# Performance work log

Hardware: AMD Instinct MI355X
Metric: run time of the kernel (lower is better)

## Reference

```python
import jax, jax.numpy as jnp
import numpy as np

PROCESSING_STEPS = 3


def setup_inputs() -> dict:
    key = jax.random.key(0)
    ks = jax.random.split(key, 6)
    N, D, G = 500000, 128, 4096
    x = jax.random.normal(ks[0], (N, D), dtype=jnp.float32)
    # torch LSTM param layout: [4*hidden, input] and [4*hidden, hidden], gates i,f,g,o
    s = 1.0 / np.sqrt(D)
    W_ih = jax.random.uniform(ks[1], (4 * D, 2 * D), minval=-s, maxval=s, dtype=jnp.float32)
    W_hh = jax.random.uniform(ks[2], (4 * D, D), minval=-s, maxval=s, dtype=jnp.float32)
    b_ih = jax.random.uniform(ks[3], (4 * D,), minval=-s, maxval=s, dtype=jnp.float32)
    b_hh = jax.random.uniform(ks[4], (4 * D,), minval=-s, maxval=s, dtype=jnp.float32)
    index = jnp.sort(jax.random.randint(ks[5], (N,), 0, G, dtype=jnp.int64))
    return {"x": x, "W_ih": W_ih, "W_hh": W_hh, "b_ih": b_ih, "b_hh": b_hh,
            "index": index, "dim_size": G}


def _lstm_cell(inp, h, c, W_ih, W_hh, b_ih, b_hh):
    gates = inp @ W_ih.T + h @ W_hh.T + (b_ih + b_hh)  # [G, 4D]
    i, f, g, o = jnp.split(gates, 4, axis=-1)
    c = jax.nn.sigmoid(f) * c + jax.nn.sigmoid(i) * jnp.tanh(g)
    h = jax.nn.sigmoid(o) * jnp.tanh(c)
    return h, c


def reference(x, W_ih, W_hh, b_ih, b_hh, index, dim_size):
    N, D = x.shape
    h = jnp.zeros((dim_size, D), dtype=x.dtype)
    c = jnp.zeros((dim_size, D), dtype=x.dtype)
    q_star = jnp.zeros((dim_size, 2 * D), dtype=x.dtype)
    for _ in range(PROCESSING_STEPS):
        h, c = _lstm_cell(q_star, h, c, W_ih, W_hh, b_ih, b_hh)
        q = h  # [G, D]
        e = jnp.sum(x * q[index], axis=-1)  # [N]
        # segment softmax (numerically stable)
        m = jax.ops.segment_max(e, index, num_segments=dim_size)
        m = jnp.where(jnp.isfinite(m), m, 0.0)  # guard empty segments
        ex = jnp.exp(e - m[index])
        s = jax.ops.segment_sum(ex, index, num_segments=dim_size)
        a = ex / jnp.maximum(s, 1e-16)[index]  # [N]
        r = jax.ops.segment_sum(a[:, None] * x, index, num_segments=dim_size)  # [G, D]
        q_star = jnp.concatenate([q, r], axis=-1)
    return q_star
```

## Files before the change

### kernel.cpp

```cpp
#include <hip/hip_runtime.h>
#include <math.h>

#define D 128

__device__ __forceinline__ float sigmoidf_(float x) { return 1.f / (1.f + __expf(-x)); }

__global__ void seg_bounds_kernel(const int* __restrict__ idx, int N, int G,
                                  int* __restrict__ seg_off) {
    int g = blockIdx.x * blockDim.x + threadIdx.x;
    if (g > G) return;
    int lo = 0, hi = N;
    while (lo < hi) {
        int mid = (lo + hi) >> 1;
        if (idx[mid] < g) lo = mid + 1; else hi = mid;
    }
    seg_off[g] = lo;
}

__global__ void prep_wc_kernel(const float* __restrict__ W_ih, const float* __restrict__ W_hh,
                               float* __restrict__ Wc) {
    int t = blockIdx.x * blockDim.x + threadIdx.x;
    if (t >= 4 * D * D) return;
    int j = t >> 7;
    int k = t & (D - 1);
    Wc[t] = W_ih[(size_t)j * (2 * D) + k] + W_hh[t];
}

__global__ void prep_bias_kernel(const float* __restrict__ b_ih, const float* __restrict__ b_hh,
                                 float* __restrict__ b_sum, float* __restrict__ h1,
                                 float* __restrict__ c1) {
    int t = threadIdx.x;
    float b = b_ih[t] + b_hh[t];
    b_sum[t] = b;
    if (t < D) {
        float bi = b_ih[t] + b_hh[t];
        float bg = b_ih[2 * D + t] + b_hh[2 * D + t];
        float bo = b_ih[3 * D + t] + b_hh[3 * D + t];
        float c = sigmoidf_(bi) * tanhf(bg);
        c1[t] = c;
        h1[t] = sigmoidf_(bo) * tanhf(c);
    }
}

__global__ void base2_kernel(const float* __restrict__ Wc, const float* __restrict__ b_sum,
                             const float* __restrict__ h1, float* __restrict__ base2) {
    __shared__ float hs[D];
    int j = blockIdx.x * 256 + threadIdx.x;
    if (threadIdx.x < D) hs[threadIdx.x] = h1[threadIdx.x];
    __syncthreads();
    float acc = 0.f;
    const float4* w4 = (const float4*)(Wc + (size_t)j * D);
#pragma unroll 8
    for (int k4 = 0; k4 < D / 4; ++k4) {
        float4 w = w4[k4];
        const float* hp = &hs[k4 * 4];
        acc += w.x * hp[0] + w.y * hp[1] + w.z * hp[2] + w.w * hp[3];
    }
    base2[j] = b_sum[j] + acc;
}

__global__ __launch_bounds__(256) void attn_kernel(
    const float* __restrict__ x,
    const int* __restrict__ seg_off,
    const float* __restrict__ q,
    int q_stride,
    float* __restrict__ r_out, int r_stride,
    int G) {
    int g = blockIdx.x;
    if (g >= G) return;
    int tid = threadIdx.x;
    int wave = tid >> 6, lane = tid & 63;
    int half = lane >> 5, col4 = lane & 31;

    __shared__ float sm[4], ss[4];
    __shared__ float sacc[4][D];

    int start = seg_off[g], end = seg_off[g + 1];
    int count = end - start;
    int chunk = (count + 3) >> 2;
    int wsr = start + wave * chunk;
    int wer = min(wsr + chunk, end);

    const float4* x4 = (const float4*)x;
    const float4* q4 = (const float4*)(q + (size_t)g * q_stride);
    float4 qv = q4[col4];

    float m = -INFINITY, s = 0.f;
    float4 acc = {0.f, 0.f, 0.f, 0.f};

    if (wsr < wer) {
        int last = wer - 1;
        int ngroups = (wer - wsr + 7) >> 3;
        for (int it = 0; it < ngroups; ++it) {
            int base = wsr + it * 8;
            int ra = min(base + 0 + half, last);
            int rb = min(base + 2 + half, last);
            int rc = min(base + 4 + half, last);
            int rd = min(base + 6 + half, last);
            float4 xa = x4[(size_t)ra * 32 + col4];
            float4 xb = x4[(size_t)rb * 32 + col4];
            float4 xc = x4[(size_t)rc * 32 + col4];
            float4 xd = x4[(size_t)rd * 32 + col4];

            float pa = xa.x * qv.x + xa.y * qv.y + xa.z * qv.z + xa.w * qv.w;
            float pb = xb.x * qv.x + xb.y * qv.y + xb.z * qv.z + xb.w * qv.w;
            float pc = xc.x * qv.x + xc.y * qv.y + xc.z * qv.z + xc.w * qv.w;
            float pd = xd.x * qv.x + xd.y * qv.y + xd.z * qv.z + xd.w * qv.w;
#pragma unroll
            for (int off = 1; off < 32; off <<= 1) {
                pa += __shfl_xor(pa, off);
                pb += __shfl_xor(pb, off);
                pc += __shfl_xor(pc, off);
                pd += __shfl_xor(pd, off);
            }
            float oa = __shfl_xor(pa, 32);
            float ob = __shfl_xor(pb, 32);
            float oc = __shfl_xor(pc, 32);
            float od = __shfl_xor(pd, 32);
            float pae = half ? oa : pa, pao = half ? pa : oa;
            float pbe = half ? ob : pb, pbo = half ? pb : ob;
            float pce = half ? oc : pc, pco = half ? pc : oc;
            float pde = half ? od : pd, pdo = half ? pd : od;
            pae = (base + 0 < wer) ? pae : -INFINITY;
            pao = (base + 1 < wer) ? pao : -INFINITY;
            pbe = (base + 2 < wer) ? pbe : -INFINITY;
            pbo = (base + 3 < wer) ? pbo : -INFINITY;
            pce = (base + 4 < wer) ? pce : -INFINITY;
            pco = (base + 5 < wer) ? pco : -INFINITY;
            pde = (base + 6 < wer) ? pde : -INFINITY;
            pdo = (base + 7 < wer) ? pdo : -INFINITY;

            float mn = fmaxf(fmaxf(fmaxf(pae, pao), fmaxf(pbe, pbo)),
                             fmaxf(fmaxf(pce, pco), fmaxf(pde, pdo)));
            mn = fmaxf(m, mn);
            float al = __expf(m - mn);
            float wae = __expf(pae - mn), wao = __expf(pao - mn);
            float wbe = __expf(pbe - mn), wbo = __expf(pbo - mn);
            float wce = __expf(pce - mn), wco = __expf(pco - mn);
            float wde = __expf(pde - mn), wdo = __expf(pdo - mn);
            float sg = (wae + wao) + (wbe + wbo) + ((wce + wco) + (wde + wdo));
            s = s * al + sg;
            float wsa = half ? wao : wae;
            float wsb = half ? wbo : wbe;
            float wsc = half ? wco : wce;
            float wsd = half ? wdo : wde;
            float tx = wsa * xa.x + wsb * xb.x + wsc * xc.x + wsd * xd.x;
            float ty = wsa * xa.y + wsb * xb.y + wsc * xc.y + wsd * xd.y;
            float tz = wsa * xa.z + wsb * xb.z + wsc * xc.z + wsd * xd.z;
            float tw = wsa * xa.w + wsb * xb.w + wsc * xc.w + wsd * xd.w;
            acc.x = acc.x * al + tx;
            acc.y = acc.y * al + ty;
            acc.z = acc.z * al + tz;
            acc.w = acc.w * al + tw;
            m = mn;
        }
    }
    acc.x += __shfl_xor(acc.x, 32);
    acc.y += __shfl_xor(acc.y, 32);
    acc.z += __shfl_xor(acc.z, 32);
    acc.w += __shfl_xor(acc.w, 32);

    if (lane == 0) { sm[wave] = m; ss[wave] = s; }
    if (half == 0) *(float4*)&sacc[wave][col4 * 4] = acc;
    __syncthreads();

    if (tid < D) {
        float m0 = sm[0], m1 = sm[1], m2 = sm[2], m3 = sm[3];
        float mstar = fmaxf(fmaxf(m0, m1), fmaxf(m2, m3));
        float r = 0.f;
        if (mstar > -INFINITY) {
            float e0 = __expf(m0 - mstar), e1 = __expf(m1 - mstar);
            float e2 = __expf(m2 - mstar), e3 = __expf(m3 - mstar);
            float stot = ss[0] * e0 + ss[1] * e1 + ss[2] * e2 + ss[3] * e3;
            float at = sacc[0][tid] * e0 + sacc[1][tid] * e1
                     + sacc[2][tid] * e2 + sacc[3][tid] * e3;
            r = at / fmaxf(stot, 1e-16f);
        }
        r_out[(size_t)g * r_stride + tid] = r;
    }
}

__global__ __launch_bounds__(256) void gates_gemm_kernel(
    const float* __restrict__ A1, const float* __restrict__ W1,
    const float* __restrict__ A2, const float* __restrict__ W2, int sW2,
    const float* __restrict__ bias, float* __restrict__ gates) {
    __shared__ float As[16][132];
    __shared__ float Ws[16][132];
    int t = threadIdx.x;
    int tx = t & 15, ty = t >> 4;
    int g0 = blockIdx.x * 128, j0 = blockIdx.y * 128;
    int lr = t >> 1;
    int lk = (t & 1) * 8;

    float acc[8][8];
#pragma unroll
    for (int i = 0; i < 8; ++i)
#pragma unroll
        for (int j = 0; j < 8; ++j) acc[i][j] = 0.f;

    for (int phase = 0; phase < 2; ++phase) {
        const float* A = phase ? A2 : A1;
        if (A == nullptr) continue;
        const float* W = phase ? W2 : W1;
        int sW = phase ? sW2 : D;
        for (int kk = 0; kk < D; kk += 16) {
            float4 a0 = *(const float4*)&A[(size_t)(g0 + lr) * D + kk + lk];
            float4 a1 = *(const float4*)&A[(size_t)(g0 + lr) * D + kk + lk + 4];
            float4 w0 = *(const float4*)&W[(size_t)(j0 + lr) * sW + kk + lk];
            float4 w1 = *(const float4*)&W[(size_t)(j0 + lr) * sW + kk + lk + 4];
            __syncthreads();
            As[lk + 0][lr] = a0.x; As[lk + 1][lr] = a0.y; As[lk + 2][lr] = a0.z; As[lk + 3][lr] = a0.w;
            As[lk + 4][lr] = a1.x; As[lk + 5][lr] = a1.y; As[lk + 6][lr] = a1.z; As[lk + 7][lr] = a1.w;
            Ws[lk + 0][lr] = w0.x; Ws[lk + 1][lr] = w0.y; Ws[lk + 2][lr] = w0.z; Ws[lk + 3][lr] = w0.w;
            Ws[lk + 4][lr] = w1.x; Ws[lk + 5][lr] = w1.y; Ws[lk + 6][lr] = w1.z; Ws[lk + 7][lr] = w1.w;
            __syncthreads();
#pragma unroll
            for (int k = 0; k < 16; ++k) {
                float4 a0v = *(const float4*)&As[k][ty * 8];
                float4 a1v = *(const float4*)&As[k][ty * 8 + 4];
                float4 b0v = *(const float4*)&Ws[k][tx * 8];
                float4 b1v = *(const float4*)&Ws[k][tx * 8 + 4];
                float av[8] = {a0v.x, a0v.y, a0v.z, a0v.w, a1v.x, a1v.y, a1v.z, a1v.w};
                float bv[8] = {b0v.x, b0v.y, b0v.z, b0v.w, b1v.x, b1v.y, b1v.z, b1v.w};
#pragma unroll
                for (int i = 0; i < 8; ++i)
#pragma unroll
                    for (int j = 0; j < 8; ++j)
                        acc[i][j] = fmaf(av[i], bv[j], acc[i][j]);
            }
        }
    }
#pragma unroll
    for (int i = 0; i < 8; ++i) {
        size_t row = (size_t)(g0 + ty * 8 + i);
        float4 o0, o1;
        int jb = j0 + tx * 8;
        o0.x = acc[i][0] + bias[jb + 0]; o0.y = acc[i][1] + bias[jb + 1];
        o0.z = acc[i][2] + bias[jb + 2]; o0.w = acc[i][3] + bias[jb + 3];
        o1.x = acc[i][4] + bias[jb + 4]; o1.y = acc[i][5] + bias[jb + 5];
        o1.z = acc[i][6] + bias[jb + 6]; o1.w = acc[i][7] + bias[jb + 7];
        *(float4*)&gates[row * 512 + jb] = o0;
        *(float4*)&gates[row * 512 + jb + 4] = o1;
    }
}

__global__ void cell_kernel(const float* __restrict__ gates,
                            const float* __restrict__ c_prev, int c_stride,
                            float* __restrict__ c_out,
                            float* __restrict__ h_out, int h_stride,
                            int total) {
    int t = blockIdx.x * blockDim.x + threadIdx.x;
    if (t >= total) return;
    int g = t >> 7, k = t & (D - 1);
    const float* grow = gates + (size_t)g * 512;
    float ig = grow[k];
    float fg = grow[D + k];
    float gg = grow[2 * D + k];
    float og = grow[3 * D + k];
    float cp = c_prev[(size_t)g * c_stride + k];
    float c = sigmoidf_(fg) * cp + sigmoidf_(ig) * tanhf(gg);
    float h = sigmoidf_(og) * tanhf(c);
    c_out[t] = c;
    h_out[(size_t)g * h_stride + k] = h;
}

extern "C" void kernel_launch(void* const* d_in, const int* in_sizes, int n_in,
                              void* d_out, int out_size, void* d_ws, size_t ws_size,
                              hipStream_t stream) {
    const float* x      = (const float*)d_in[0];
    const float* W_ih   = (const float*)d_in[1];
    const float* W_hh   = (const float*)d_in[2];
    const float* b_ih   = (const float*)d_in[3];
    const float* b_hh   = (const float*)d_in[4];
    const int*   index  = (const int*)d_in[5];
    int N = in_sizes[5];
    int G = out_size / (2 * D);
    float* out = (float*)d_out;

    float* ws = (float*)d_ws;
    float* Wc     = ws;
    float* b_sum  = Wc + 4 * D * D;
    float* h1     = b_sum + 4 * D;
    float* c1     = h1 + D;
    float* base2  = c1 + D;
    float* r1     = base2 + 4 * D;
    float* h2     = r1 + (size_t)G * D;
    float* c2     = h2 + (size_t)G * D;
    float* r2     = c2 + (size_t)G * D;
    float* gatesb = r2 + (size_t)G * D;
    int* seg_off  = (int*)(gatesb + (size_t)G * 4 * D);
    float* c3     = r1;

    seg_bounds_kernel<<<(G + 1 + 255) / 256, 256, 0, stream>>>(index, N, G, seg_off);
    prep_wc_kernel<<<(4 * D * D + 255) / 256, 256, 0, stream>>>(W_ih, W_hh, Wc);
    prep_bias_kernel<<<1, 512, 0, stream>>>(b_ih, b_hh, b_sum, h1, c1);
    base2_kernel<<<2, 256, 0, stream>>>(Wc, b_sum, h1, base2);

    attn_kernel<<<G, 256, 0, stream>>>(x, seg_off, h1, 0, r1, D, G);

    gates_gemm_kernel<<<dim3(G / 128, 4), 256, 0, stream>>>(
        nullptr, Wc, r1, W_ih + D, 2 * D, base2, gatesb);
    cell_kernel<<<(G * D + 255) / 256, 256, 0, stream>>>(gatesb, c1, 0, c2, h2, D, G * D);
    attn_kernel<<<G, 256, 0, stream>>>(x, seg_off, h2, D, r2, D, G);

    gates_gemm_kernel<<<dim3(G / 128, 4), 256, 0, stream>>>(
        h2, Wc, r2, W_ih + D, 2 * D, b_sum, gatesb);
    cell_kernel<<<(G * D + 255) / 256, 256, 0, stream>>>(gatesb, c2, D, c3, out, 2 * D, G * D);
    attn_kernel<<<G, 256, 0, stream>>>(x, seg_off, out, 2 * D, out + D, 2 * D, G);
}
```

Baseline: 523.1 us.

## Fuse prep kernels into one launch and shrink gates GEMM tiles to 64x64

Merges the segment-bounds, combined-weight, and bias/initial-state kernels into one prep kernel, so fewer launches happen. It drops the precomputed base2 vector and instead runs the first-step GEMM with a broadcast h1 row (stride 0), which adds a small amount of GEMM work. The gates GEMM moves from 128x128 tiles with 8x8 per-thread to 64x64 tiles with 4x4 per-thread and K-step 32, giving 4x more blocks for better CU occupancy on 4096 rows at the cost of lower register-level reuse.

```diff
diff --git a/kernel.cpp b/kernel.cpp
--- a/kernel.cpp
+++ b/kernel.cpp
@@ -5,67 +5,44 @@
 
 __device__ __forceinline__ float sigmoidf_(float x) { return 1.f / (1.f + __expf(-x)); }
 
-__global__ void seg_bounds_kernel(const int* __restrict__ idx, int N, int G,
-                                  int* __restrict__ seg_off) {
-    int g = blockIdx.x * blockDim.x + threadIdx.x;
-    if (g > G) return;
-    int lo = 0, hi = N;
-    while (lo < hi) {
-        int mid = (lo + hi) >> 1;
-        if (idx[mid] < g) lo = mid + 1; else hi = mid;
-    }
-    seg_off[g] = lo;
-}
-
-__global__ void prep_wc_kernel(const float* __restrict__ W_ih, const float* __restrict__ W_hh,
-                               float* __restrict__ Wc) {
-    int t = blockIdx.x * blockDim.x + threadIdx.x;
-    if (t >= 4 * D * D) return;
-    int j = t >> 7;
-    int k = t & (D - 1);
-    Wc[t] = W_ih[(size_t)j * (2 * D) + k] + W_hh[t];
-}
-
-__global__ void prep_bias_kernel(const float* __restrict__ b_ih, const float* __restrict__ b_hh,
-                                 float* __restrict__ b_sum, float* __restrict__ h1,
-                                 float* __restrict__ c1) {
-    int t = threadIdx.x;
-    float b = b_ih[t] + b_hh[t];
-    b_sum[t] = b;
-    if (t < D) {
-        float bi = b_ih[t] + b_hh[t];
-        float bg = b_ih[2 * D + t] + b_hh[2 * D + t];
-        float bo = b_ih[3 * D + t] + b_hh[3 * D + t];
-        float c = sigmoidf_(bi) * tanhf(bg);
-        c1[t] = c;
-        h1[t] = sigmoidf_(bo) * tanhf(c);
-    }
-}
-
-__global__ void base2_kernel(const float* __restrict__ Wc, const float* __restrict__ b_sum,
-                             const float* __restrict__ h1, float* __restrict__ base2) {
-    __shared__ float hs[D];
-    int j = blockIdx.x * 256 + threadIdx.x;
-    if (threadIdx.x < D) hs[threadIdx.x] = h1[threadIdx.x];
-    __syncthreads();
-    float acc = 0.f;
-    const float4* w4 = (const float4*)(Wc + (size_t)j * D);
-#pragma unroll 8
-    for (int k4 = 0; k4 < D / 4; ++k4) {
-        float4 w = w4[k4];
-        const float* hp = &hs[k4 * 4];
-        acc += w.x * hp[0] + w.y * hp[1] + w.z * hp[2] + w.w * hp[3];
-    }
-    base2[j] = b_sum[j] + acc;
+__global__ void prep_kernel(const float* __restrict__ W_ih, const float* __restrict__ W_hh,
+                            const float* __restrict__ b_ih, const float* __restrict__ b_hh,
+                            const int* __restrict__ idx, int N, int G,
+                            float* __restrict__ Wc, int* __restrict__ seg_off,
+                            float* __restrict__ b_sum, float* __restrict__ h1,
+                            float* __restrict__ c1) {
+    int b = blockIdx.x, t = threadIdx.x;
+    if (b < 256) {
+        int i = b * 256 + t;
+        int j = i >> 7, k = i & (D - 1);
+        Wc[i] = W_ih[(size_t)j * (2 * D) + k] + W_hh[i];
+    } else if (b < 273) {
+        int g = (b - 256) * 256 + t;
+        if (g <= G) {
+            int lo = 0, hi = N;
+            while (lo < hi) {
+                int mid = (lo + hi) >> 1;
+                if (idx[mid] < g) lo = mid + 1; else hi = mid;
+            }
+            seg_off[g] = lo;
+        }
+    } else {
+        for (int i = t; i < 4 * D; i += 256) b_sum[i] = b_ih[i] + b_hh[i];
+        if (t < D) {
+            float bi = b_ih[t] + b_hh[t];
+            float bg = b_ih[2 * D + t] + b_hh[2 * D + t];
+            float bo = b_ih[3 * D + t] + b_hh[3 * D + t];
+            float c = sigmoidf_(bi) * tanhf(bg);
+            c1[t] = c;
+            h1[t] = sigmoidf_(bo) * tanhf(c);
+        }
+    }
 }
 
 __global__ __launch_bounds__(256) void attn_kernel(
-    const float* __restrict__ x,
-    const int* __restrict__ seg_off,
-    const float* __restrict__ q,
-    int q_stride,
-    float* __restrict__ r_out, int r_stride,
-    int G) {
+    const float* __restrict__ x, const int* __restrict__ seg_off,
+    const float* __restrict__ q, int q_stride,
+    float* __restrict__ r_out, int r_stride, int G) {
     int g = blockIdx.x;
     if (g >= G) return;
     int tid = threadIdx.x;
@@ -181,31 +158,34 @@
 }
 
 __global__ __launch_bounds__(256) void gates_gemm_kernel(
-    const float* __restrict__ A1, const float* __restrict__ W1,
-    const float* __restrict__ A2, const float* __restrict__ W2, int sW2,
-    const float* __restrict__ bias, float* __restrict__ gates) {
-    __shared__ float As[16][132];
-    __shared__ float Ws[16][132];
+    const float* __restrict__ A1, int sA1,
+    const float* __restrict__ W1,
+    const float* __restrict__ A2,
+    const float* __restrict__ W2, int sW2,
+    const float* __restrict__ bias,
+    float* __restrict__ gates) {
+    __shared__ float As[32][72];
+    __shared__ float Ws[32][72];
     int t = threadIdx.x;
     int tx = t & 15, ty = t >> 4;
-    int g0 = blockIdx.x * 128, j0 = blockIdx.y * 128;
-    int lr = t >> 1;
-    int lk = (t & 1) * 8;
-
-    float acc[8][8];
-#pragma unroll
-    for (int i = 0; i < 8; ++i)
-#pragma unroll
-        for (int j = 0; j < 8; ++j) acc[i][j] = 0.f;
+    int g0 = blockIdx.x * 64, j0 = blockIdx.y * 64;
+    int lr = t & 63;
+    int lk = (t >> 6) * 8;
+
+    float acc[4][4];
+#pragma unroll
+    for (int i = 0; i < 4; ++i)
+#pragma unroll
+        for (int j = 0; j < 4; ++j) acc[i][j] = 0.f;
 
     for (int phase = 0; phase < 2; ++phase) {
         const float* A = phase ? A2 : A1;
-        if (A == nullptr) continue;
+        int sA = phase ? D : sA1;
         const float* W = phase ? W2 : W1;
         int sW = phase ? sW2 : D;
-        for (int kk = 0; kk < D; kk += 16) {
-            float4 a0 = *(const float4*)&A[(size_t)(g0 + lr) * D + kk + lk];
-            float4 a1 = *(const float4*)&A[(size_t)(g0 + lr) * D + kk + lk + 4];
+        for (int kk = 0; kk < D; kk += 32) {
+            float4 a0 = *(const float4*)&A[(size_t)(g0 + lr) * sA + kk + lk];
+            float4 a1 = *(const float4*)&A[(size_t)(g0 + lr) * sA + kk + lk + 4];
             float4 w0 = *(const float4*)&W[(size_t)(j0 + lr) * sW + kk + lk];
             float4 w1 = *(const float4*)&W[(size_t)(j0 + lr) * sW + kk + lk + 4];
             __syncthreads();
@@ -215,32 +195,29 @@
             Ws[lk + 4][lr] = w1.x; Ws[lk + 5][lr] = w1.y; Ws[lk + 6][lr] = w1.z; Ws[lk + 7][lr] = w1.w;
             __syncthreads();
 #pragma unroll
-            for (int k = 0; k < 16; ++k) {
-                float4 a0v = *(const float4*)&As[k][ty * 8];
-                float4 a1v = *(const float4*)&As[k][ty * 8 + 4];
-                float4 b0v = *(const float4*)&Ws[k][tx * 8];
-                float4 b1v = *(const float4*)&Ws[k][tx * 8 + 4];
-                float av[8] = {a0v.x, a0v.y, a0v.z, a0v.w, a1v.x, a1v.y, a1v.z, a1v.w};
-                float bv[8] = {b0v.x, b0v.y, b0v.z, b0v.w, b1v.x, b1v.y, b1v.z, b1v.w};
-#pragma unroll
-                for (int i = 0; i < 8; ++i)
-#pragma unroll
-                    for (int j = 0; j < 8; ++j)
-                        acc[i][j] = fmaf(av[i], bv[j], acc[i][j]);
+            for (int k = 0; k < 32; ++k) {
+                float4 av = *(const float4*)&As[k][ty * 4];
+                float4 bv = *(const float4*)&Ws[k][tx * 4];
+                float aa[4] = {av.x, av.y, av.z, av.w};
+                float bb[4] = {bv.x, bv.y, bv.z, bv.w};
+#pragma unroll
+                for (int i = 0; i < 4; ++i)
+#pragma unroll
+                    for (int j = 0; j < 4; ++j)
+                        acc[i][j] = fmaf(aa[i], bb[j], acc[i][j]);
             }
         }
     }
 #pragma unroll
-    for (int i = 0; i < 8; ++i) {
-        size_t row = (size_t)(g0 + ty * 8 + i);
-        float4 o0, o1;
-        int jb = j0 + tx * 8;
-        o0.x = acc[i][0] + bias[jb + 0]; o0.y = acc[i][1] + bias[jb + 1];
-        o0.z = acc[i][2] + bias[jb + 2]; o0.w = acc[i][3] + bias[jb + 3];
-        o1.x = acc[i][4] + bias[jb + 4]; o1.y = acc[i][5] + bias[jb + 5];
-        o1.z = acc[i][6] + bias[jb + 6]; o1.w = acc[i][7] + bias[jb + 7];
-        *(float4*)&gates[row * 512 + jb] = o0;
-        *(float4*)&gates[row * 512 + jb + 4] = o1;
+    for (int i = 0; i < 4; ++i) {
+        size_t row = (size_t)(g0 + ty * 4 + i);
+        int jb = j0 + tx * 4;
+        float4 o;
+        o.x = acc[i][0] + bias[jb + 0];
+        o.y = acc[i][1] + bias[jb + 1];
+        o.z = acc[i][2] + bias[jb + 2];
+        o.w = acc[i][3] + bias[jb + 3];
+        *(float4*)&gates[row * 512 + jb] = o;
     }
 }
 
@@ -282,8 +259,7 @@
     float* b_sum  = Wc + 4 * D * D;
     float* h1     = b_sum + 4 * D;
     float* c1     = h1 + D;
-    float* base2  = c1 + D;
-    float* r1     = base2 + 4 * D;
+    float* r1     = c1 + D;
     float* h2     = r1 + (size_t)G * D;
     float* c2     = h2 + (size_t)G * D;
     float* r2     = c2 + (size_t)G * D;
@@ -291,20 +267,18 @@
     int* seg_off  = (int*)(gatesb + (size_t)G * 4 * D);
     float* c3     = r1;
 
-    seg_bounds_kernel<<<(G + 1 + 255) / 256, 256, 0, stream>>>(index, N, G, seg_off);
-    prep_wc_kernel<<<(4 * D * D + 255) / 256, 256, 0, stream>>>(W_ih, W_hh, Wc);
-    prep_bias_kernel<<<1, 512, 0, stream>>>(b_ih, b_hh, b_sum, h1, c1);
-    base2_kernel<<<2, 256, 0, stream>>>(Wc, b_sum, h1, base2);
+    prep_kernel<<<274, 256, 0, stream>>>(W_ih, W_hh, b_ih, b_hh, index, N, G,
+                                         Wc, seg_off, b_sum, h1, c1);
 
     attn_kernel<<<G, 256, 0, stream>>>(x, seg_off, h1, 0, r1, D, G);
 
-    gates_gemm_kernel<<<dim3(G / 128, 4), 256, 0, stream>>>(
-        nullptr, Wc, r1, W_ih + D, 2 * D, base2, gatesb);
+    gates_gemm_kernel<<<dim3(G / 64, 8), 256, 0, stream>>>(
+        h1, 0, Wc, r1, W_ih + D, 2 * D, b_sum, gatesb);
     cell_kernel<<<(G * D + 255) / 256, 256, 0, stream>>>(gatesb, c1, 0, c2, h2, D, G * D);
     attn_kernel<<<G, 256, 0, stream>>>(x, seg_off, h2, D, r2, D, G);
 
-    gates_gemm_kernel<<<dim3(G / 128, 4), 256, 0, stream>>>(
-        h2, Wc, r2, W_ih + D, 2 * D, b_sum, gatesb);
+    gates_gemm_kernel<<<dim3(G / 64, 8), 256, 0, stream>>>(
+        h2, D, Wc, r2, W_ih + D, 2 * D, b_sum, gatesb);
     cell_kernel<<<(G * D + 255) / 256, 256, 0, stream>>>(gatesb, c2, D, c3, out, 2 * D, G * D);
     attn_kernel<<<G, 256, 0, stream>>>(x, seg_off, out, 2 * D, out + D, 2 * D, G);
 }
```

Result: faster. 494.6 us (-5.5%).
